# Optimization experiments

Measured on AMD Instinct MI355X. Metric: run time of the kernel, lower is better.

## Reference

```python
import jax, jax.numpy as jnp
import numpy as np

FACTOR = 1.0
KERNEL = 3
PAD = 1
STRIDE = 1


def setup_inputs() -> dict:
    key = jax.random.key(0)
    ks = jax.random.split(key, 7)
    B_, Cin, Cout, L, CODE = 32, 128, 128, 4096, 2
    return {
        "input": jax.random.normal(ks[0], (B_, Cin, L), dtype=jnp.float32),
        "codes": jax.random.normal(ks[1], (B_, CODE, CODE), dtype=jnp.float32),
        "weight": jax.random.normal(ks[2], (Cout, Cin, KERNEL), dtype=jnp.float32) * 0.05,
        "A": jax.random.normal(ks[3], (Cin, CODE, KERNEL), dtype=jnp.float32) * 0.05,
        "B": jax.random.normal(ks[4], (Cout, CODE, KERNEL), dtype=jnp.float32) * 0.05,
        "bias": jax.random.normal(ks[5], (Cout,), dtype=jnp.float32) * 0.05,
        "bias_context": jax.random.normal(ks[6], (CODE, Cout), dtype=jnp.float32) * 0.05,
    }


def reference(input, codes, weight, A, B, bias, bias_context):
    # Hypernetwork-generated per-sample conv weights (low-rank via codes)
    w = jnp.einsum('ick,bcr->birk', A, codes)            # (b, in, code, k)
    context_w = jnp.einsum('birk,ork->boik', w, B)       # (b, out, in, k)
    combined_weight = weight + FACTOR * context_w        # (b, out, in, k)

    diag = jnp.diagonal(codes, axis1=-2, axis2=-1)       # (b, code)
    context_bias = diag @ bias_context                   # (b, out)
    combined_bias = bias + FACTOR * context_bias         # (b, out)

    # circular padding along spatial axis
    padded = jnp.pad(input, ((0, 0), (0, 0), (PAD, PAD)), mode='wrap')
    L_out = (input.shape[-1] + 2 * PAD - KERNEL) // STRIDE + 1
    # windowed view: (b, in, L_out, k) via k shifted slices (k is tiny, loop ok)
    windows = jnp.stack([padded[:, :, j:j + L_out * STRIDE:STRIDE] for j in range(KERNEL)], axis=-1)
    out = jnp.einsum('bihw,boiw->boh', windows, combined_weight)
    return out + combined_bias[..., None]
```

## Files before the change

### kernel.cpp

```cpp
#include <hip/hip_runtime.h>
#include <hip/hip_bf16.h>
#include <stdint.h>
#include <stddef.h>

#define L_LEN 4096
#define CIN   128
#define COUT  128
#define NB    32
#define KTOT  384
#define TN    128
#define ROWS  (TN + 2)

typedef __bf16 bf16x8 __attribute__((ext_vector_type(8)));
typedef float  f32x4  __attribute__((ext_vector_type(4)));

__device__ __forceinline__ uint16_t f2bf(float f) {
    union { float f; uint32_t u; } v; v.f = f;
    return (uint16_t)((v.u + 0x7fffu + ((v.u >> 16) & 1u)) >> 16);
}

__device__ __forceinline__ void load_lds16(const void* g, void* l) {
    __builtin_amdgcn_global_load_lds(
        (const __attribute__((address_space(1))) void*)g,
        (__attribute__((address_space(3))) void*)l, 16, 0, 0);
}

__global__ __launch_bounds__(256) void geps_combine(
    const float* __restrict__ codes, const float* __restrict__ weight,
    const float* __restrict__ Amat,  const float* __restrict__ Bmat,
    const float* __restrict__ bias,  const float* __restrict__ bias_ctx,
    uint16_t* __restrict__ Wc, float* __restrict__ cbias)
{
    int tid = blockIdx.x * 256 + threadIdx.x;
    if (tid < NB * COUT * KTOT) {
        int b   = tid / (COUT * KTOT);
        int rem = tid % (COUT * KTOT);
        int o   = rem / KTOT;
        int kp  = rem % KTOT;
        int k   = kp >> 7;
        int i   = kp & 127;
        float cw = 0.f;
        #pragma unroll
        for (int c = 0; c < 2; ++c) {
            float a = Amat[i * 6 + c * 3 + k];
            #pragma unroll
            for (int r = 0; r < 2; ++r)
                cw += a * codes[b * 4 + c * 2 + r] * Bmat[o * 6 + r * 3 + k];
        }
        float val = weight[o * 384 + i * 3 + k] + cw;
        Wc[tid] = f2bf(val);
    }
    if (tid < NB * COUT) {
        int b = tid >> 7, o = tid & 127;
        float cb = bias[o];
        #pragma unroll
        for (int c = 0; c < 2; ++c)
            cb += codes[b * 4 + c * 2 + c] * bias_ctx[c * 128 + o];
        cbias[tid] = cb;
    }
}

__global__ __launch_bounds__(256, 3) void geps_conv(
    const float* __restrict__ in, const uint16_t* __restrict__ Wc,
    const float* __restrict__ cbias, float* __restrict__ out)
{
    __shared__ uint16_t __attribute__((aligned(16))) Xt[ROWS * 128];
    __shared__ uint16_t __attribute__((aligned(16))) Asm[128 * 32];
    __shared__ float cb[COUT];

    const int tid  = threadIdx.x;
    const int b    = blockIdx.y;
    const int h0   = blockIdx.x * TN;
    const int lane = tid & 63;
    const int wid  = tid >> 6;

    if (tid < COUT) cb[tid] = cbias[b * COUT + tid];

    const float* inb = in + (size_t)b * CIN * L_LEN;
    for (int idx = tid; idx < 64 * ROWS; idx += 256) {
        int p  = idx / ROWS;
        int r  = idx - p * ROWS;
        int gh = (h0 - 1 + r) & (L_LEN - 1);
        float x0 = inb[(size_t)(2 * p    ) * L_LEN + gh];
        float x1 = inb[(size_t)(2 * p + 1) * L_LEN + gh];
        uint32_t v = (uint32_t)f2bf(x0) | ((uint32_t)f2bf(x1) << 16);
        int chunk = (p >> 2) ^ (r & 15);
        *(uint32_t*)&Xt[r * 128 + (chunk << 3) + ((2 * p) & 7)] = v;
    }

    const int mq  = (wid & 1) * 64;
    const int nq  = (wid >> 1) * 64;
    const int m16 = lane & 15;
    const int q   = lane >> 4;

    f32x4 acc[4][4];
    #pragma unroll
    for (int a = 0; a < 4; ++a)
        #pragma unroll
        for (int c = 0; c < 4; ++c) acc[a][c] = 0.0f;

    const uint16_t* WcB = Wc + (size_t)b * COUT * KTOT;

    for (int t = 0; t < 12; ++t) {
        __syncthreads();
        #pragma unroll
        for (int p2 = 0; p2 < 2; ++p2) {
            int qq = (p2 * 4 + wid) * 64 + lane;
            int o  = qq >> 2;
            int c4 = qq & 3;
            load_lds16(WcB + o * KTOT + t * 32 + c4 * 8,
                       &Asm[(p2 * 4 + wid) * 512]);
        }
        __syncthreads();

        const int k   = t >> 2;
        const int i0c = (t & 3) * 4;
        bf16x8 af[4], bf[4];
        #pragma unroll
        for (int mt = 0; mt < 4; ++mt) {
            int o = mq + mt * 16 + m16;
            af[mt] = *(const bf16x8*)&Asm[o * 32 + q * 8];
        }
        #pragma unroll
        for (int nt = 0; nt < 4; ++nt) {
            int r  = nq + nt * 16 + m16 + k;
            int ch = (i0c + q) ^ (r & 15);
            bf[nt] = *(const bf16x8*)&Xt[r * 128 + (ch << 3)];
        }
        #pragma unroll
        for (int mt = 0; mt < 4; ++mt)
            #pragma unroll
            for (int nt = 0; nt < 4; ++nt)
                acc[mt][nt] = __builtin_amdgcn_mfma_f32_16x16x32_bf16(
                    af[mt], bf[nt], acc[mt][nt], 0, 0, 0);
    }

    float* outb = out + (size_t)b * COUT * L_LEN + h0;
    #pragma unroll
    for (int mt = 0; mt < 4; ++mt) {
        #pragma unroll
        for (int reg = 0; reg < 4; ++reg) {
            int o = mq + mt * 16 + q * 4 + reg;
            float bv = cb[o];
            float* orow = outb + (size_t)o * L_LEN;
            #pragma unroll
            for (int nt = 0; nt < 4; ++nt) {
                int h = nq + nt * 16 + m16;
                orow[h] = acc[mt][nt][reg] + bv;
            }
        }
    }
}

extern "C" void kernel_launch(void* const* d_in, const int* in_sizes, int n_in,
                              void* d_out, int out_size, void* d_ws, size_t ws_size,
                              hipStream_t stream) {
    const float* input    = (const float*)d_in[0];
    const float* codes    = (const float*)d_in[1];
    const float* weight   = (const float*)d_in[2];
    const float* Amat     = (const float*)d_in[3];
    const float* Bmat     = (const float*)d_in[4];
    const float* bias     = (const float*)d_in[5];
    const float* bias_ctx = (const float*)d_in[6];
    float* out = (float*)d_out;

    uint16_t* Wc    = (uint16_t*)d_ws;
    float*    cbias = (float*)((char*)d_ws + (size_t)NB * COUT * KTOT * 2);

    geps_combine<<<dim3((NB * COUT * KTOT) / 256), 256, 0, stream>>>(
        codes, weight, Amat, Bmat, bias, bias_ctx, Wc, cbias);
    geps_conv<<<dim3(L_LEN / TN, NB), 256, 0, stream>>>(input, Wc, cbias, out);
}
```

Before: 145.6 us.

## Load weight fragments directly from global and vectorize input staging

The conv kernel no longer stages per-batch weight tiles through shared memory with two barriers per k-step. Each wave now reads its bf16 weight fragments straight from global memory (L2-resident), the k-loop is fully unrolled, and only one barrier remains. Input staging switches from scalar strided loads to float4 loads along the spatial axis, with a separate path for the two halo rows. Occupancy bounds rise from 3 to 4 blocks per SM since LDS use drops, at the cost of redundant global weight reads across waves and higher register pressure.

```diff
diff --git a/kernel.cpp b/kernel.cpp
--- a/kernel.cpp
+++ b/kernel.cpp
@@ -18,11 +18,8 @@
     union { float f; uint32_t u; } v; v.f = f;
     return (uint16_t)((v.u + 0x7fffu + ((v.u >> 16) & 1u)) >> 16);
 }
-
-__device__ __forceinline__ void load_lds16(const void* g, void* l) {
-    __builtin_amdgcn_global_load_lds(
-        (const __attribute__((address_space(1))) void*)g,
-        (__attribute__((address_space(3))) void*)l, 16, 0, 0);
+__device__ __forceinline__ uint32_t pack2(float lo, float hi) {
+    return (uint32_t)f2bf(lo) | ((uint32_t)f2bf(hi) << 16);
 }
 
 __global__ __launch_bounds__(256) void geps_combine(
@@ -60,12 +57,11 @@
     }
 }
 
-__global__ __launch_bounds__(256, 3) void geps_conv(
+__global__ __launch_bounds__(256, 4) void geps_conv(
     const float* __restrict__ in, const uint16_t* __restrict__ Wc,
     const float* __restrict__ cbias, float* __restrict__ out)
 {
     __shared__ uint16_t __attribute__((aligned(16))) Xt[ROWS * 128];
-    __shared__ uint16_t __attribute__((aligned(16))) Asm[128 * 32];
     __shared__ float cb[COUT];
 
     const int tid  = threadIdx.x;
@@ -77,15 +73,35 @@
     if (tid < COUT) cb[tid] = cbias[b * COUT + tid];
 
     const float* inb = in + (size_t)b * CIN * L_LEN;
-    for (int idx = tid; idx < 64 * ROWS; idx += 256) {
-        int p  = idx / ROWS;
-        int r  = idx - p * ROWS;
-        int gh = (h0 - 1 + r) & (L_LEN - 1);
-        float x0 = inb[(size_t)(2 * p    ) * L_LEN + gh];
+
+    #pragma unroll
+    for (int it = 0; it < 8; ++it) {
+        int task = it * 256 + tid;
+        int p    = task >> 5;
+        int qd   = task & 31;
+        const float* r0 = inb + (size_t)(2 * p) * L_LEN + h0 + 4 * qd;
+        const float4 a  = *(const float4*)r0;
+        const float4 c  = *(const float4*)(r0 + L_LEN);
+        const int off   = (2 * p) & 7;
+        const int pc    = p >> 2;
+        const float av[4] = {a.x, a.y, a.z, a.w};
+        const float cv[4] = {c.x, c.y, c.z, c.w};
+        #pragma unroll
+        for (int j = 0; j < 4; ++j) {
+            int r = 1 + 4 * qd + j;
+            int chunk = pc ^ (r & 15);
+            *(uint32_t*)&Xt[r * 128 + (chunk << 3) + off] = pack2(av[j], cv[j]);
+        }
+    }
+    if (tid < 128) {
+        int p    = tid & 63;
+        int side = tid >> 6;
+        int r    = side ? (ROWS - 1) : 0;
+        int gh   = (h0 - 1 + r) & (L_LEN - 1);
+        float x0 = inb[(size_t)(2 * p)     * L_LEN + gh];
         float x1 = inb[(size_t)(2 * p + 1) * L_LEN + gh];
-        uint32_t v = (uint32_t)f2bf(x0) | ((uint32_t)f2bf(x1) << 16);
         int chunk = (p >> 2) ^ (r & 15);
-        *(uint32_t*)&Xt[r * 128 + (chunk << 3) + ((2 * p) & 7)] = v;
+        *(uint32_t*)&Xt[r * 128 + (chunk << 3) + ((2 * p) & 7)] = pack2(x0, x1);
     }
 
     const int mq  = (wid & 1) * 64;
@@ -101,25 +117,17 @@
 
     const uint16_t* WcB = Wc + (size_t)b * COUT * KTOT;
 
+    __syncthreads();
+
+    #pragma unroll
     for (int t = 0; t < 12; ++t) {
-        __syncthreads();
-        #pragma unroll
-        for (int p2 = 0; p2 < 2; ++p2) {
-            int qq = (p2 * 4 + wid) * 64 + lane;
-            int o  = qq >> 2;
-            int c4 = qq & 3;
-            load_lds16(WcB + o * KTOT + t * 32 + c4 * 8,
-                       &Asm[(p2 * 4 + wid) * 512]);
-        }
-        __syncthreads();
-
         const int k   = t >> 2;
         const int i0c = (t & 3) * 4;
         bf16x8 af[4], bf[4];
         #pragma unroll
         for (int mt = 0; mt < 4; ++mt) {
             int o = mq + mt * 16 + m16;
-            af[mt] = *(const bf16x8*)&Asm[o * 32 + q * 8];
+            af[mt] = *(const bf16x8*)(WcB + (size_t)o * KTOT + t * 32 + q * 8);
         }
         #pragma unroll
         for (int nt = 0; nt < 4; ++nt) {
```

Measured after the change: 145.6 us. No clear change (-0.0%).
